# Performance work log

Hardware: AMD Instinct MI355X
Metric: run time of the kernel (lower is better)

Reference implementation:

```python
import jax, jax.numpy as jnp
import numpy as np

K = 7          # involution kernel size
G = 16         # groups = channels // group_channels = 256 // 16
BN_EPS = 1e-3  # Keras BatchNormalization default epsilon


def setup_inputs() -> dict:
    key = jax.random.key(0)
    ks = jax.random.split(key, 6)
    B, H, W, C = 4, 56, 56, 256
    Cr = C // 4                      # reduction_ratio = 4
    x = jax.random.normal(ks[0], (B, H, W, C), dtype=jnp.float32)
    w_reduce = jax.random.normal(ks[1], (C, Cr), dtype=jnp.float32) * (1.0 / np.sqrt(C))
    gamma = jnp.ones((Cr,), dtype=jnp.float32)
    beta = jnp.zeros((Cr,), dtype=jnp.float32)
    mean = jax.random.normal(ks[2], (Cr,), dtype=jnp.float32) * 0.1
    var = jax.random.uniform(ks[3], (Cr,), dtype=jnp.float32) + 0.5
    w_span = jax.random.normal(ks[4], (Cr, K * K * G), dtype=jnp.float32) * (1.0 / np.sqrt(Cr))
    b_span = jnp.zeros((K * K * G,), dtype=jnp.float32)
    return {"x": x, "w_reduce": w_reduce, "gamma": gamma, "beta": beta,
            "mean": mean, "var": var, "w_span": w_span, "b_span": b_span}


def reference(x, w_reduce, gamma, beta, mean, var, w_span, b_span):
    B, H, W, C = x.shape
    Cg = C // G  # channels per group
    # kernel generation branch: 1x1 conv -> BN (inference) -> ReLU -> 1x1 conv
    r = jnp.einsum('bhwc,cd->bhwd', x, w_reduce)
    r = jax.nn.relu((r - mean) * (gamma / jnp.sqrt(var + BN_EPS)) + beta)
    kgen = jnp.einsum('bhwd,de->bhwe', r, w_span) + b_span      # (B,H,W,K*K*G)
    kgen = kgen.reshape(B, H, W, G, K * K)
    # im2col with SAME padding (stride=1, pad (K-1)//2 symmetric), depth order (kh, kw, C)
    p = (K - 1) // 2
    xp = jnp.pad(x, ((0, 0), (p, p), (p, p), (0, 0)))
    patches = jnp.stack([xp[:, i:i + H, j:j + W, :]
                         for i in range(K) for j in range(K)], axis=3)  # (B,H,W,K*K,C)
    patches = patches.reshape(B, H, W, K * K, G, Cg)
    # per-pixel, per-group weighted reduction over the K*K window
    out = jnp.einsum('bhwgk,bhwkgc->bhwgc', kgen, patches)
    return out.reshape(B, H, W, C)
```

## Files before the change

kernel.cpp:

```cpp
#include <hip/hip_runtime.h>
#include <hip/hip_bf16.h>
#include <stdint.h>

#define B_   4
#define H_   56
#define W_   56
#define C_   256
#define CR   64
#define G_   16
#define CG   16
#define KS   7
#define KK   49
#define PADR 3
#define NPX  (B_*H_*W_)

typedef __attribute__((ext_vector_type(8))) short bf16x8;
typedef __attribute__((ext_vector_type(4))) float f32x4;
typedef __attribute__((ext_vector_type(2))) float f32x2;

__device__ __forceinline__ uint32_t f2bf(float f) {
    uint32_t x = __float_as_uint(f);
    return (x + 0x7fffu + ((x >> 16) & 1u)) >> 16;
}
__device__ __forceinline__ uint32_t pkbf(float a, float b) {
    union { __hip_bfloat162 h; uint32_t u; } c;
    c.h = __float22bfloat162_rn(make_float2(a, b));
    return c.u;
}
__device__ __forceinline__ float blo(uint32_t w) { return __uint_as_float(w << 16); }
__device__ __forceinline__ float bhi(uint32_t w) { return __uint_as_float(w & 0xffff0000u); }

union U4V { uint4 u; bf16x8 v; };

__global__ __launch_bounds__(256) void k0_prepack(
        const float* __restrict__ wr, const float* __restrict__ wspan,
        const float* __restrict__ gamma, const float* __restrict__ beta,
        const float* __restrict__ mean, const float* __restrict__ var,
        uint16_t* __restrict__ wrp, uint16_t* __restrict__ wpp,
        float* __restrict__ scale, float* __restrict__ shift) {
    int idx = blockIdx.x * 256 + threadIdx.x;
    {
        int j = idx & 7, lane = (idx >> 3) & 63, nb = (idx >> 9) & 3,
            kb = (idx >> 11) & 1, g = idx >> 12;
        int k = kb * 32 + (lane >> 4) * 8 + j;
        int n = nb * 16 + (lane & 15);
        float v = (n < KK) ? wspan[k * (KK * G_) + g * KK + n] : 0.f;
        wpp[idx] = (uint16_t)f2bf(v);
    }
    if (idx < 16384) {
        int j = idx & 7, lane = (idx >> 3) & 63, nb = (idx >> 9) & 3, kb = idx >> 11;
        int k = kb * 32 + (lane >> 4) * 8 + j;
        int n = nb * 16 + (lane & 15);
        wrp[idx] = (uint16_t)f2bf(wr[k * CR + n]);
    }
    if (idx < CR) {
        float s = gamma[idx] * rsqrtf(var[idx] + 1e-3f);
        scale[idx] = s;
        shift[idx] = beta[idx] - mean[idx] * s;
    }
}

__global__ __launch_bounds__(256) void k1_reduce(
        const float* __restrict__ x, const uint16_t* __restrict__ wrp,
        const float* __restrict__ scale, const float* __restrict__ shift,
        uint16_t* __restrict__ r, uint16_t* __restrict__ xbf) {
    int tid = threadIdx.x;
    int lane = tid & 63, w = tid >> 6;
    int mt = blockIdx.x * 4 + w;
    int pix = mt * 16 + (lane & 15);
    int ko = (lane >> 4) * 8;
    const float* xrow = x + (size_t)pix * C_ + ko;
    f32x4 acc[4] = {{0,0,0,0},{0,0,0,0},{0,0,0,0},{0,0,0,0}};
    for (int kb = 0; kb < 8; ++kb) {
        float4 a0 = *(const float4*)(xrow + kb * 32);
        float4 a1 = *(const float4*)(xrow + kb * 32 + 4);
        U4V af;
        af.u = make_uint4(pkbf(a0.x, a0.y), pkbf(a0.z, a0.w),
                          pkbf(a1.x, a1.y), pkbf(a1.z, a1.w));
        *(uint4*)(xbf + (size_t)pix * C_ + ko + kb * 32) = af.u;
        const uint16_t* wb = wrp + kb * 2048 + lane * 8;
        #pragma unroll
        for (int nb = 0; nb < 4; ++nb) {
            bf16x8 bf_ = *(const bf16x8*)(wb + nb * 512);
            acc[nb] = __builtin_amdgcn_mfma_f32_16x16x32_bf16(af.v, bf_, acc[nb], 0, 0, 0);
        }
    }
    int rq = (lane >> 4) * 4;
    #pragma unroll
    for (int nb = 0; nb < 4; ++nb) {
        int d = nb * 16 + (lane & 15);
        float s = scale[d], sh = shift[d];
        #pragma unroll
        for (int rg = 0; rg < 4; ++rg) {
            float v = fmaf(acc[nb][rg], s, sh);
            v = v > 0.f ? v : 0.f;
            r[(size_t)(mt * 16 + rq + rg) * CR + d] = (uint16_t)f2bf(v);
        }
    }
}

#define TS   14
#define HS   20
#define XSW  16
#define KGW  56

__global__ __launch_bounds__(256, 4) void k2_involution(
        const uint16_t* __restrict__ xbf, const uint16_t* __restrict__ r,
        const uint16_t* __restrict__ wpp, const float* __restrict__ bspan,
        float* __restrict__ out) {
    __shared__ __align__(16) uint16_t xs[HS * HS * XSW];
    __shared__ __align__(16) uint16_t kg[196 * KGW];

    int tid  = threadIdx.x;
    int tile = blockIdx.x, g = blockIdx.y, b = blockIdx.z;
    int ty0 = (tile >> 2) * TS, tx0 = (tile & 3) * TS;

    #pragma unroll
    for (int pass = 0; pass < 2; ++pass) {
        int i = tid + pass * 256;
        if (i < HS * HS) {
            int py = i / HS, px = i % HS;
            int gy = ty0 + py - PADR, gx = tx0 + px - PADR;
            uint4 wA = make_uint4(0, 0, 0, 0), wB = wA;
            if (gy >= 0 && gy < H_ && gx >= 0 && gx < W_) {
                const uint16_t* xp = xbf + (((size_t)(b * H_ + gy)) * W_ + gx) * C_ + g * CG;
                wA = *(const uint4*)(xp);
                wB = *(const uint4*)(xp + 8);
            }
            uint16_t* dst = xs + i * XSW;
            *(uint4*)(dst + 0) = wA;
            *(uint4*)(dst + 8) = wB;
        }
    }

    int lane = tid & 63, w = tid >> 6;
    bf16x8 bfr[2][4];
    const uint16_t* wb = wpp + g * 4096 + lane * 8;
    #pragma unroll
    for (int kb = 0; kb < 2; ++kb)
        #pragma unroll
        for (int nb = 0; nb < 4; ++nb)
            bfr[kb][nb] = *(const bf16x8*)(wb + kb * 2048 + nb * 512);
    float bias[4];
    #pragma unroll
    for (int nb = 0; nb < 4; ++nb) {
        int n = nb * 16 + (lane & 15);
        bias[nb] = (n < KK) ? bspan[g * KK + n] : 0.f;
    }
    for (int mi = 0; mi < 4; ++mi) {
        int mt = mi * 4 + w;
        if (mt < 13) {
            int m  = mt * 16 + (lane & 15);
            int mm = m < 196 ? m : 195;
            int ly = mm / TS, lx = mm % TS;
            size_t pix = ((size_t)(b * H_ + ty0 + ly)) * W_ + (tx0 + lx);
            const uint16_t* rp = r + pix * CR + (lane >> 4) * 8;
            bf16x8 a0 = *(const bf16x8*)(rp);
            bf16x8 a1 = *(const bf16x8*)(rp + 32);
            f32x4 acc[4];
            #pragma unroll
            for (int nb = 0; nb < 4; ++nb)
                acc[nb] = (f32x4){bias[nb], bias[nb], bias[nb], bias[nb]};
            #pragma unroll
            for (int nb = 0; nb < 4; ++nb) {
                acc[nb] = __builtin_amdgcn_mfma_f32_16x16x32_bf16(a0, bfr[0][nb], acc[nb], 0, 0, 0);
                acc[nb] = __builtin_amdgcn_mfma_f32_16x16x32_bf16(a1, bfr[1][nb], acc[nb], 0, 0, 0);
            }
            int row = mt * 16 + (lane >> 4) * 4;
            if (row < 196) {
                #pragma unroll
                for (int nb = 0; nb < 4; ++nb) {
                    int n = nb * 16 + (lane & 15);
                    if (n < KK) {
                        int slot = n + n / 7;
                        #pragma unroll
                        for (int rg = 0; rg < 4; ++rg)
                            kg[(row + rg) * KGW + slot] = (uint16_t)f2bf(acc[nb][rg]);
                    }
                }
            }
        }
    }
    __syncthreads();

    if (tid < 196) {
        int p = tid >> 1, h = tid & 1;
        int ty = p / 7, tx = (p % 7) * 2;
        const uint16_t* kgL = kg + (ty * TS + tx) * KGW;
        const uint16_t* kgR = kgL + KGW;

        f32x2 accL[4] = {{0,0},{0,0},{0,0},{0,0}};
        f32x2 accR[4] = {{0,0},{0,0},{0,0},{0,0}};
        #pragma unroll
        for (int kh = 0; kh < KS; ++kh) {
            uint4 aL = *(const uint4*)(kgL + kh * 8);
            uint4 aR = *(const uint4*)(kgR + kh * 8);
            const uint32_t kwL[4] = {aL.x, aL.y, aL.z, aL.w};
            const uint32_t kwR[4] = {aR.x, aR.y, aR.z, aR.w};
            const uint16_t* xrow = xs + ((ty + kh) * HS + tx) * XSW + h * 8;
            #pragma unroll
            for (int j = 0; j < 8; ++j) {
                uint4 xw = *(const uint4*)(xrow + j * XSW);
                float kvL = 0.f, kvR = 0.f;
                if (j < 7) kvL = (j & 1) ? bhi(kwL[j >> 1]) : blo(kwL[j >> 1]);
                if (j > 0) { int t = j - 1; kvR = (t & 1) ? bhi(kwR[t >> 1]) : blo(kwR[t >> 1]); }
                f32x2 kL = {kvL, kvL}, kR = {kvR, kvR};
                f32x2 x0 = {blo(xw.x), bhi(xw.x)};
                f32x2 x1 = {blo(xw.y), bhi(xw.y)};
                f32x2 x2 = {blo(xw.z), bhi(xw.z)};
                f32x2 x3 = {blo(xw.w), bhi(xw.w)};
                accL[0] = __builtin_elementwise_fma(kL, x0, accL[0]);
                accL[1] = __builtin_elementwise_fma(kL, x1, accL[1]);
                accL[2] = __builtin_elementwise_fma(kL, x2, accL[2]);
                accL[3] = __builtin_elementwise_fma(kL, x3, accL[3]);
                accR[0] = __builtin_elementwise_fma(kR, x0, accR[0]);
                accR[1] = __builtin_elementwise_fma(kR, x1, accR[1]);
                accR[2] = __builtin_elementwise_fma(kR, x2, accR[2]);
                accR[3] = __builtin_elementwise_fma(kR, x3, accR[3]);
            }
        }
        size_t pixL = ((size_t)(b * H_ + ty0 + ty)) * W_ + (tx0 + tx);
        float* opL = out + pixL * C_ + g * CG + h * 8;
        float* opR = opL + C_;
        *(float4*)(opL + 0) = make_float4(accL[0].x, accL[0].y, accL[1].x, accL[1].y);
        *(float4*)(opL + 4) = make_float4(accL[2].x, accL[2].y, accL[3].x, accL[3].y);
        *(float4*)(opR + 0) = make_float4(accR[0].x, accR[0].y, accR[1].x, accR[1].y);
        *(float4*)(opR + 4) = make_float4(accR[2].x, accR[2].y, accR[3].x, accR[3].y);
    }
}

extern "C" void kernel_launch(void* const* d_in, const int* in_sizes, int n_in,
                              void* d_out, int out_size, void* d_ws, size_t ws_size,
                              hipStream_t stream) {
    const float* x        = (const float*)d_in[0];
    const float* w_reduce = (const float*)d_in[1];
    const float* gamma    = (const float*)d_in[2];
    const float* beta     = (const float*)d_in[3];
    const float* mean     = (const float*)d_in[4];
    const float* var      = (const float*)d_in[5];
    const float* w_span   = (const float*)d_in[6];
    const float* b_span   = (const float*)d_in[7];
    float* out = (float*)d_out;

    uint8_t* ws = (uint8_t*)d_ws;
    uint16_t* r_ws  = (uint16_t*)(ws + 0);
    uint16_t* wrp   = (uint16_t*)(ws + 1605632);
    uint16_t* wpp   = (uint16_t*)(ws + 1638400);
    float*    scale = (float*)   (ws + 1769472);
    float*    shift = (float*)   (ws + 1769728);
    uint16_t* xbf   = (uint16_t*)(ws + 1769984);

    hipLaunchKernelGGL(k0_prepack, dim3(256), dim3(256), 0, stream,
                       w_reduce, w_span, gamma, beta, mean, var,
                       wrp, wpp, scale, shift);
    hipLaunchKernelGGL(k1_reduce, dim3(NPX / 64), dim3(256), 0, stream,
                       x, wrp, scale, shift, r_ws, xbf);
    hipLaunchKernelGGL(k2_involution, dim3(16, 16, B_), dim3(256), 0, stream,
                       xbf, r_ws, wpp, b_span, out);
}
```

Baseline: 98.46 us.

## Fuse weight prepack into reduce kernel and read fp32 x directly in involution

```diff
diff --git a/kernel.cpp b/kernel.cpp
--- a/kernel.cpp
+++ b/kernel.cpp
@@ -32,53 +32,58 @@
 
 union U4V { uint4 u; bf16x8 v; };
 
-__global__ __launch_bounds__(256) void k0_prepack(
-        const float* __restrict__ wr, const float* __restrict__ wspan,
+__global__ __launch_bounds__(256) void k1_reduce(
+        const float* __restrict__ x, const float* __restrict__ wreduce,
+        const float* __restrict__ wspan,
         const float* __restrict__ gamma, const float* __restrict__ beta,
         const float* __restrict__ mean, const float* __restrict__ var,
-        uint16_t* __restrict__ wrp, uint16_t* __restrict__ wpp,
-        float* __restrict__ scale, float* __restrict__ shift) {
-    int idx = blockIdx.x * 256 + threadIdx.x;
-    {
-        int j = idx & 7, lane = (idx >> 3) & 63, nb = (idx >> 9) & 3,
-            kb = (idx >> 11) & 1, g = idx >> 12;
-        int k = kb * 32 + (lane >> 4) * 8 + j;
-        int n = nb * 16 + (lane & 15);
-        float v = (n < KK) ? wspan[k * (KK * G_) + g * KK + n] : 0.f;
-        wpp[idx] = (uint16_t)f2bf(v);
-    }
-    if (idx < 16384) {
-        int j = idx & 7, lane = (idx >> 3) & 63, nb = (idx >> 9) & 3, kb = idx >> 11;
-        int k = kb * 32 + (lane >> 4) * 8 + j;
-        int n = nb * 16 + (lane & 15);
-        wrp[idx] = (uint16_t)f2bf(wr[k * CR + n]);
-    }
-    if (idx < CR) {
-        float s = gamma[idx] * rsqrtf(var[idx] + 1e-3f);
-        scale[idx] = s;
-        shift[idx] = beta[idx] - mean[idx] * s;
-    }
-}
-
-__global__ __launch_bounds__(256) void k1_reduce(
-        const float* __restrict__ x, const uint16_t* __restrict__ wrp,
-        const float* __restrict__ scale, const float* __restrict__ shift,
-        uint16_t* __restrict__ r, uint16_t* __restrict__ xbf) {
+        uint16_t* __restrict__ r, uint16_t* __restrict__ wpp) {
+    __shared__ __align__(16) uint16_t wrpLds[16384];
     int tid = threadIdx.x;
     int lane = tid & 63, w = tid >> 6;
-    int mt = blockIdx.x * 4 + w;
+
+    #pragma unroll
+    for (int q = 0; q < 8; ++q) {
+        int f  = q * 256 + tid;
+        int fl = f & 63, nb = (f >> 6) & 3, kb = f >> 8;
+        int k0 = kb * 32 + (fl >> 4) * 8;
+        int n  = nb * 16 + (fl & 15);
+        uint32_t wd[4];
+        #pragma unroll
+        for (int jj = 0; jj < 4; ++jj)
+            wd[jj] = pkbf(wreduce[(k0 + 2 * jj) * CR + n],
+                          wreduce[(k0 + 2 * jj + 1) * CR + n]);
+        *(uint4*)(wrpLds + f * 8) = make_uint4(wd[0], wd[1], wd[2], wd[3]);
+    }
+    if (blockIdx.x < 128 && tid < 64) {
+        int f  = blockIdx.x * 64 + tid;
+        int fl = f & 63, nb = (f >> 6) & 3, kb = (f >> 8) & 1, g = f >> 9;
+        int k0 = kb * 32 + (fl >> 4) * 8;
+        int n  = nb * 16 + (fl & 15);
+        uint32_t wd[4];
+        #pragma unroll
+        for (int jj = 0; jj < 4; ++jj) {
+            float a = (n < KK) ? wspan[(k0 + 2 * jj) * (KK * G_) + g * KK + n] : 0.f;
+            float c = (n < KK) ? wspan[(k0 + 2 * jj + 1) * (KK * G_) + g * KK + n] : 0.f;
+            wd[jj] = pkbf(a, c);
+        }
+        *(uint4*)(wpp + (size_t)f * 8) = make_uint4(wd[0], wd[1], wd[2], wd[3]);
+    }
+    __syncthreads();
+
+    int mt  = blockIdx.x * 4 + w;
     int pix = mt * 16 + (lane & 15);
-    int ko = (lane >> 4) * 8;
+    int ko  = (lane >> 4) * 8;
     const float* xrow = x + (size_t)pix * C_ + ko;
     f32x4 acc[4] = {{0,0,0,0},{0,0,0,0},{0,0,0,0},{0,0,0,0}};
+    #pragma unroll
     for (int kb = 0; kb < 8; ++kb) {
         float4 a0 = *(const float4*)(xrow + kb * 32);
         float4 a1 = *(const float4*)(xrow + kb * 32 + 4);
         U4V af;
         af.u = make_uint4(pkbf(a0.x, a0.y), pkbf(a0.z, a0.w),
                           pkbf(a1.x, a1.y), pkbf(a1.z, a1.w));
-        *(uint4*)(xbf + (size_t)pix * C_ + ko + kb * 32) = af.u;
-        const uint16_t* wb = wrp + kb * 2048 + lane * 8;
+        const uint16_t* wb = wrpLds + kb * 2048 + lane * 8;
         #pragma unroll
         for (int nb = 0; nb < 4; ++nb) {
             bf16x8 bf_ = *(const bf16x8*)(wb + nb * 512);
@@ -89,7 +94,8 @@
     #pragma unroll
     for (int nb = 0; nb < 4; ++nb) {
         int d = nb * 16 + (lane & 15);
-        float s = scale[d], sh = shift[d];
+        float s  = gamma[d] * rsqrtf(var[d] + 1e-3f);
+        float sh = beta[d] - mean[d] * s;
         #pragma unroll
         for (int rg = 0; rg < 4; ++rg) {
             float v = fmaf(acc[nb][rg], s, sh);
@@ -101,14 +107,14 @@
 
 #define TS   14
 #define HS   20
-#define XSW  16
+#define XSP  21
 #define KGW  56
 
 __global__ __launch_bounds__(256, 4) void k2_involution(
-        const uint16_t* __restrict__ xbf, const uint16_t* __restrict__ r,
+        const float* __restrict__ x, const uint16_t* __restrict__ r,
         const uint16_t* __restrict__ wpp, const float* __restrict__ bspan,
         float* __restrict__ out) {
-    __shared__ __align__(16) uint16_t xs[HS * HS * XSW];
+    __shared__ __align__(16) uint16_t xs[420 * 16];
     __shared__ __align__(16) uint16_t kg[196 * KGW];
 
     int tid  = threadIdx.x;
@@ -123,11 +129,17 @@
             int gy = ty0 + py - PADR, gx = tx0 + px - PADR;
             uint4 wA = make_uint4(0, 0, 0, 0), wB = wA;
             if (gy >= 0 && gy < H_ && gx >= 0 && gx < W_) {
-                const uint16_t* xp = xbf + (((size_t)(b * H_ + gy)) * W_ + gx) * C_ + g * CG;
-                wA = *(const uint4*)(xp);
-                wB = *(const uint4*)(xp + 8);
-            }
-            uint16_t* dst = xs + i * XSW;
+                const float* xp = x + (((size_t)(b * H_ + gy)) * W_ + gx) * C_ + g * CG;
+                float4 a0 = *(const float4*)(xp);
+                float4 a1 = *(const float4*)(xp + 4);
+                float4 a2 = *(const float4*)(xp + 8);
+                float4 a3 = *(const float4*)(xp + 12);
+                wA = make_uint4(pkbf(a0.x, a0.y), pkbf(a0.z, a0.w),
+                                pkbf(a1.x, a1.y), pkbf(a1.z, a1.w));
+                wB = make_uint4(pkbf(a2.x, a2.y), pkbf(a2.z, a2.w),
+                                pkbf(a3.x, a3.y), pkbf(a3.z, a3.w));
+            }
+            uint16_t* dst = xs + (py * XSP + px) * 16;
             *(uint4*)(dst + 0) = wA;
             *(uint4*)(dst + 8) = wB;
         }
@@ -174,8 +186,11 @@
                     if (n < KK) {
                         int slot = n + n / 7;
                         #pragma unroll
-                        for (int rg = 0; rg < 4; ++rg)
-                            kg[(row + rg) * KGW + slot] = (uint16_t)f2bf(acc[nb][rg]);
+                        for (int rg = 0; rg < 4; ++rg) {
+                            int rr  = row + rg;
+                            int rho = (rr >> 1) + (rr & 1) * 98;
+                            kg[rho * KGW + slot] = (uint16_t)f2bf(acc[nb][rg]);
+                        }
                     }
                 }
             }
@@ -186,8 +201,8 @@
     if (tid < 196) {
         int p = tid >> 1, h = tid & 1;
         int ty = p / 7, tx = (p % 7) * 2;
-        const uint16_t* kgL = kg + (ty * TS + tx) * KGW;
-        const uint16_t* kgR = kgL + KGW;
+        const uint16_t* kgL = kg + p * KGW;
+        const uint16_t* kgR = kg + (98 + p) * KGW;
 
         f32x2 accL[4] = {{0,0},{0,0},{0,0},{0,0}};
         f32x2 accR[4] = {{0,0},{0,0},{0,0},{0,0}};
@@ -197,26 +212,31 @@
             uint4 aR = *(const uint4*)(kgR + kh * 8);
             const uint32_t kwL[4] = {aL.x, aL.y, aL.z, aL.w};
             const uint32_t kwR[4] = {aR.x, aR.y, aR.z, aR.w};
-            const uint16_t* xrow = xs + ((ty + kh) * HS + tx) * XSW + h * 8;
+            const uint16_t* xrow = xs + ((ty + kh) * XSP + tx) * 16 + h * 8;
             #pragma unroll
             for (int j = 0; j < 8; ++j) {
-                uint4 xw = *(const uint4*)(xrow + j * XSW);
-                float kvL = 0.f, kvR = 0.f;
-                if (j < 7) kvL = (j & 1) ? bhi(kwL[j >> 1]) : blo(kwL[j >> 1]);
-                if (j > 0) { int t = j - 1; kvR = (t & 1) ? bhi(kwR[t >> 1]) : blo(kwR[t >> 1]); }
-                f32x2 kL = {kvL, kvL}, kR = {kvR, kvR};
+                uint4 xw = *(const uint4*)(xrow + j * 16);
                 f32x2 x0 = {blo(xw.x), bhi(xw.x)};
                 f32x2 x1 = {blo(xw.y), bhi(xw.y)};
                 f32x2 x2 = {blo(xw.z), bhi(xw.z)};
                 f32x2 x3 = {blo(xw.w), bhi(xw.w)};
-                accL[0] = __builtin_elementwise_fma(kL, x0, accL[0]);
-                accL[1] = __builtin_elementwise_fma(kL, x1, accL[1]);
-                accL[2] = __builtin_elementwise_fma(kL, x2, accL[2]);
-                accL[3] = __builtin_elementwise_fma(kL, x3, accL[3]);
-                accR[0] = __builtin_elementwise_fma(kR, x0, accR[0]);
-                accR[1] = __builtin_elementwise_fma(kR, x1, accR[1]);
-                accR[2] = __builtin_elementwise_fma(kR, x2, accR[2]);
-                accR[3] = __builtin_elementwise_fma(kR, x3, accR[3]);
+                if (j < 7) {
+                    float kv = (j & 1) ? bhi(kwL[j >> 1]) : blo(kwL[j >> 1]);
+                    f32x2 kL = {kv, kv};
+                    accL[0] = __builtin_elementwise_fma(kL, x0, accL[0]);
+                    accL[1] = __builtin_elementwise_fma(kL, x1, accL[1]);
+                    accL[2] = __builtin_elementwise_fma(kL, x2, accL[2]);
+                    accL[3] = __builtin_elementwise_fma(kL, x3, accL[3]);
+                }
+                if (j > 0) {
+                    int t = j - 1;
+                    float kv = (t & 1) ? bhi(kwR[t >> 1]) : blo(kwR[t >> 1]);
+                    f32x2 kR = {kv, kv};
+                    accR[0] = __builtin_elementwise_fma(kR, x0, accR[0]);
+                    accR[1] = __builtin_elementwise_fma(kR, x1, accR[1]);
+                    accR[2] = __builtin_elementwise_fma(kR, x2, accR[2]);
+                    accR[3] = __builtin_elementwise_fma(kR, x3, accR[3]);
+                }
             }
         }
         size_t pixL = ((size_t)(b * H_ + ty0 + ty)) * W_ + (tx0 + tx);
@@ -243,18 +263,11 @@
     float* out = (float*)d_out;
 
     uint8_t* ws = (uint8_t*)d_ws;
-    uint16_t* r_ws  = (uint16_t*)(ws + 0);
-    uint16_t* wrp   = (uint16_t*)(ws + 1605632);
-    uint16_t* wpp   = (uint16_t*)(ws + 1638400);
-    float*    scale = (float*)   (ws + 1769472);
-    float*    shift = (float*)   (ws + 1769728);
-    uint16_t* xbf   = (uint16_t*)(ws + 1769984);
-
-    hipLaunchKernelGGL(k0_prepack, dim3(256), dim3(256), 0, stream,
-                       w_reduce, w_span, gamma, beta, mean, var,
-                       wrp, wpp, scale, shift);
+    uint16_t* r_ws = (uint16_t*)(ws + 0);
+    uint16_t* wpp  = (uint16_t*)(ws + 1605632);
+
     hipLaunchKernelGGL(k1_reduce, dim3(NPX / 64), dim3(256), 0, stream,
-                       x, wrp, scale, shift, r_ws, xbf);
+                       x, w_reduce, w_span, gamma, beta, mean, var, r_ws, wpp);
     hipLaunchKernelGGL(k2_involution, dim3(16, 16, B_), dim3(256), 0, stream,
-                       xbf, r_ws, wpp, b_span, out);
-}
+                       x, r_ws, wpp, b_span, out);
+}
```

Result: slower. 102.9 us (+4.5%).
